# Kernel tuning notes

Hardware: AMD Instinct MI355X
Metric: run time of the kernel (lower is better)

## Reference

```python
import jax, jax.numpy as jnp
import numpy as np

WS = (2, 7, 7)   # window size (d, h, w)
NH = 4           # num heads
EPS = 1e-5       # LayerNorm eps (torch default)


def _rel_index():
    wd, wh, ww = WS
    coords = np.stack(np.meshgrid(np.arange(wd), np.arange(wh), np.arange(ww), indexing='ij'))  # (3,wd,wh,ww)
    cf = coords.reshape(3, -1)                      # (3, N)
    rel = cf[:, :, None] - cf[:, None, :]           # (3, N, N)
    rel = rel.transpose(1, 2, 0).astype(np.int64)   # (N, N, 3)
    rel[..., 0] += wd - 1
    rel[..., 1] += wh - 1
    rel[..., 2] += ww - 1
    rel[..., 0] *= (2 * wh - 1) * (2 * ww - 1)
    rel[..., 1] *= (2 * ww - 1)
    return jnp.asarray(rel.sum(-1), dtype=jnp.int32)  # (N, N)


def setup_inputs() -> dict:
    key = jax.random.key(0)
    ks = jax.random.split(key, 6)
    C, CH = 128, 512
    TBL = (2 * WS[0] - 1) * (2 * WS[1] - 1) * (2 * WS[2] - 1)  # 507
    rn = lambda k, s, sc=0.02: jax.random.normal(k, s, jnp.float32) * sc
    return {
        'x': jax.random.normal(ks[0], (2, 8, 56, 56, C), jnp.float32),
        'norm1_w': jnp.ones((C,), jnp.float32), 'norm1_b': jnp.zeros((C,), jnp.float32),
        'qkv_w': rn(ks[1], (3 * C, C)), 'qkv_b': jnp.zeros((3 * C,), jnp.float32),
        'bias_table': rn(ks[2], (TBL, NH)),
        'proj_w': rn(ks[3], (C, C)), 'proj_b': jnp.zeros((C,), jnp.float32),
        'norm2_w': jnp.ones((C,), jnp.float32), 'norm2_b': jnp.zeros((C,), jnp.float32),
        'fc1_w': rn(ks[4], (CH, C)), 'fc1_b': jnp.zeros((CH,), jnp.float32),
        'fc2_w': rn(ks[5], (C, CH)), 'fc2_b': jnp.zeros((C,), jnp.float32),
        'rel_index': _rel_index(),
    }


def _layernorm(x, w, b):
    m = jnp.mean(x, axis=-1, keepdims=True)
    v = jnp.mean(jnp.square(x - m), axis=-1, keepdims=True)
    return (x - m) * jax.lax.rsqrt(v + EPS) * w + b


def reference(x, norm1_w, norm1_b, qkv_w, qkv_b, bias_table, proj_w, proj_b,
              norm2_w, norm2_b, fc1_w, fc1_b, fc2_w, fc2_b, rel_index):
    B, D, H, W, C = x.shape
    wd, wh, ww = WS
    N = wd * wh * ww
    hd = C // NH

    shortcut = x
    xn = _layernorm(x, norm1_w, norm1_b)
    # window partition: (B,D,H,W,C) -> (B*nW, N, C)
    xw = xn.reshape(B, D // wd, wd, H // wh, wh, W // ww, ww, C)
    xw = xw.transpose(0, 1, 3, 5, 2, 4, 6, 7).reshape(-1, N, C)
    B_ = xw.shape[0]

    qkv = (xw @ qkv_w.T + qkv_b).reshape(B_, N, 3, NH, hd).transpose(2, 0, 3, 1, 4)
    q, k, v = qkv[0] * (hd ** -0.5), qkv[1], qkv[2]   # (B_, NH, N, hd)
    attn = jnp.einsum('bhnd,bhmd->bhnm', q, k)
    bias = bias_table[rel_index.reshape(-1)].reshape(N, N, NH).transpose(2, 0, 1)  # (NH,N,N)
    attn = jax.nn.softmax(attn + bias[None], axis=-1)
    out = jnp.einsum('bhnm,bhmd->bhnd', attn, v).transpose(0, 2, 1, 3).reshape(B_, N, C)
    out = out @ proj_w.T + proj_b

    # window reverse: (B*nW, N, C) -> (B,D,H,W,C)
    xr = out.reshape(B, D // wd, H // wh, W // ww, wd, wh, ww, C)
    xr = xr.transpose(0, 1, 4, 2, 5, 3, 6, 7).reshape(B, D, H, W, C)

    x = shortcut + xr
    h = _layernorm(x, norm2_w, norm2_b)
    h = jax.nn.gelu(h @ fc1_w.T + fc1_b, approximate=False)  # torch nn.GELU = exact erf
    return x + (h @ fc2_w.T + fc2_b)
```

## Files before the change

### kernel.cpp

```cpp
#include <hip/hip_runtime.h>
#include <hip/hip_bf16.h>

typedef __hip_bfloat16 bf16;
typedef unsigned short u16t;
typedef unsigned int u32t;
typedef __attribute__((ext_vector_type(8))) short bf16x8_t;
typedef __attribute__((ext_vector_type(4))) float f32x4_t;

#define DEVI static __device__ __forceinline__

DEVI float u2f(u32t bits) { union { u32t u; float f; } v; v.u = bits; return v.f; }
DEVI float bflo(u32t u) { return u2f((u & 0xffffu) << 16); }
DEVI float bfhi(u32t u) { return u2f(u & 0xffff0000u); }
DEVI float sh2f(short s) { return u2f(((u32t)(u16t)s) << 16); }
DEVI float bf2f(bf16 h) { return __bfloat162float(h); }
DEVI bf16 f2bf(float f) { return __float2bfloat16(f); }
DEVI u16t f2bfbits(float f) {
  bf16 h = __float2bfloat16(f);
  union { bf16 h; u16t u; } v; v.h = h; return v.u;
}

DEVI void gl_lds16(const void* g, void* l) {
  __builtin_amdgcn_global_load_lds(
      (const __attribute__((address_space(1))) unsigned int*)g,
      (__attribute__((address_space(3))) unsigned int*)l, 16, 0, 0);
}

#define TOK   50176
#define NWIN  512
#define NTOK  98
#define NHEAD 4
#define HDIM  32

__global__ __launch_bounds__(256) void cvt4_k(
    const float* __restrict__ a, const float* __restrict__ b,
    const float* __restrict__ c, const float* __restrict__ d,
    bf16* __restrict__ o) {
  int i = blockIdx.x * 256 + threadIdx.x;
  const float* s; int off;
  if (i < 49152)       { s = a; off = 0; }
  else if (i < 65536)  { s = b; off = 49152; }
  else if (i < 131072) { s = c; off = 65536; }
  else                 { s = d; off = 131072; }
  o[i] = f2bf(s[i - off]);
}

__global__ __launch_bounds__(256) void bias_k(const float* __restrict__ btab,
                                              const int* __restrict__ relidx,
                                              float* __restrict__ BmatT) {
  int idx = blockIdx.x * 256 + threadIdx.x;
  if (idx < NTOK * NTOK) {
    int i = idx / NTOK, j = idx - i * NTOK;
    int r = relidx[idx] * NHEAD;
#pragma unroll
    for (int h = 0; h < NHEAD; h++)
      BmatT[(size_t)(h * NTOK + j) * 112 + i] = btab[r + h];
  }
}

__global__ __launch_bounds__(256) void ln1_k(
    const float* __restrict__ x, const float* __restrict__ w,
    const float* __restrict__ b, bf16* __restrict__ o)
{
  const int wave = threadIdx.x >> 6, lane = threadIdx.x & 63;
  const int t = blockIdx.x * 4 + wave;
  const int c = lane << 1;
  float2 xv = *(const float2*)(x + (size_t)t * 128 + c);
  float x0 = xv.x, x1 = xv.y;
  float s = x0 + x1, ss = x0 * x0 + x1 * x1;
#pragma unroll
  for (int m = 32; m; m >>= 1) { s += __shfl_xor(s, m); ss += __shfl_xor(ss, m); }
  float mean = s * 0.0078125f;
  float var = ss * 0.0078125f - mean * mean;
  float rstd = rsqrtf(var + 1e-5f);
  float y0 = (x0 - mean) * rstd * w[c]     + b[c];
  float y1 = (x1 - mean) * rstd * w[c + 1] + b[c + 1];
  int wi = t % 56; int r = t / 56;
  int hi_ = r % 56; r /= 56;
  int di = r & 7; int bi = r >> 3;
  int nw = ((bi * 4 + (di >> 1)) * 8 + hi_ / 7) * 8 + wi / 7;
  int n  = ((di & 1) * 7 + hi_ % 7) * 7 + wi % 7;
  u32t ov = ((u32t)f2bfbits(y1) << 16) | (u32t)f2bfbits(y0);
  *(u32t*)((u16t*)o + (size_t)(nw * NTOK + n) * 128 + c) = ov;
}

__global__ __launch_bounds__(256) void ln2_k(
    const bf16* __restrict__ x, const float* __restrict__ w,
    const float* __restrict__ b, bf16* __restrict__ o)
{
  const int wave = threadIdx.x >> 6, lane = threadIdx.x & 63;
  const int t = blockIdx.x * 4 + wave;
  const int c = lane << 1;
  u32t u = *(const u32t*)((const u16t*)x + (size_t)t * 128 + c);
  float x0 = bflo(u), x1 = bfhi(u);
  float s = x0 + x1, ss = x0 * x0 + x1 * x1;
#pragma unroll
  for (int m = 32; m; m >>= 1) { s += __shfl_xor(s, m); ss += __shfl_xor(ss, m); }
  float mean = s * 0.0078125f;
  float var = ss * 0.0078125f - mean * mean;
  float rstd = rsqrtf(var + 1e-5f);
  float y0 = (x0 - mean) * rstd * w[c]     + b[c];
  float y1 = (x1 - mean) * rstd * w[c + 1] + b[c + 1];
  u32t ov = ((u32t)f2bfbits(y1) << 16) | (u32t)f2bfbits(y0);
  *(u32t*)((u16t*)o + (size_t)t * 128 + c) = ov;
}

template <int MODE, int NT16>
__global__ __launch_bounds__(256) void gemm_mfma_k(
    const bf16* __restrict__ A, const bf16* __restrict__ W,
    const float* __restrict__ bias, const float* __restrict__ resX,
    const bf16* __restrict__ resB2, bf16* __restrict__ outB,
    float* __restrict__ outF, int N, int K)
{
  __shared__ short As[128 * 64];
  __shared__ short Bs[NT16 * 16 * 64];
  const int tid = threadIdx.x;
  const int rowBase = blockIdx.y << 7;
  const int colBase = blockIdx.x * (NT16 * 16);
  const int wv = tid >> 6, lane = tid & 63;
  const int q = lane >> 4, r16 = lane & 15;
  const int mB = wv << 5;

  f32x4_t acc[2][NT16];
#pragma unroll
  for (int i = 0; i < 2; i++)
#pragma unroll
    for (int j = 0; j < NT16; j++) acc[i][j] = (f32x4_t){0.f, 0.f, 0.f, 0.f};

  for (int k0 = 0; k0 < K; k0 += 64) {
#pragma unroll
    for (int t = 0; t < 4; t++) {
      int f = tid + (t << 8);
      int row = f >> 3, cs = (f & 7) ^ (row & 7);
      gl_lds16((const u16t*)A + (size_t)(rowBase + row) * K + k0 + (cs << 3),
               &As[f << 3]);
    }
#pragma unroll
    for (int t = 0; t < NT16 / 2; t++) {
      int f = tid + (t << 8);
      int row = f >> 3, cs = (f & 7) ^ (row & 7);
      gl_lds16((const u16t*)W + (size_t)(colBase + row) * K + k0 + (cs << 3),
               &Bs[f << 3]);
    }
    __syncthreads();
#pragma unroll
    for (int ks = 0; ks < 2; ks++) {
      bf16x8_t af[2], bfr[NT16];
#pragma unroll
      for (int mt = 0; mt < 2; mt++) {
        int row = mB + (mt << 4) + r16;
        int ch = ((ks << 2) + q) ^ (row & 7);
        af[mt] = *(const bf16x8_t*)&As[(row << 6) + (ch << 3)];
      }
#pragma unroll
      for (int nt = 0; nt < NT16; nt++) {
        int row = (nt << 4) + r16;
        int ch = ((ks << 2) + q) ^ (row & 7);
        bfr[nt] = *(const bf16x8_t*)&Bs[(row << 6) + (ch << 3)];
      }
#pragma unroll
      for (int mt = 0; mt < 2; mt++)
#pragma unroll
        for (int nt = 0; nt < NT16; nt++)
          acc[mt][nt] = __builtin_amdgcn_mfma_f32_16x16x32_bf16(
              af[mt], bfr[nt], acc[mt][nt], 0, 0, 0);
    }
    __syncthreads();
  }

  float bv[NT16];
#pragma unroll
  for (int nt = 0; nt < NT16; nt++) bv[nt] = bias[colBase + (nt << 4) + r16];

  if (MODE == 3) {
#pragma unroll
    for (int mt = 0; mt < 2; mt++)
#pragma unroll
      for (int reg = 0; reg < 4; reg++) {
        int grow = rowBase + mB + (mt << 4) + (q << 2) + reg;
        size_t ob = (size_t)grow * N;
#pragma unroll
        for (int nt = 0; nt < NT16; nt++) {
          int gcol = colBase + (nt << 4) + r16;
          outF[ob + gcol] = acc[mt][nt][reg] + bv[nt] + bf2f(resB2[ob + gcol]);
        }
      }
    return;
  }

#pragma unroll
  for (int mt = 0; mt < 2; mt++)
#pragma unroll
    for (int reg = 0; reg < 4; reg++) {
      int lrow = mB + (mt << 4) + (q << 2) + reg;
#pragma unroll
      for (int nt = 0; nt < NT16; nt++) {
        float v = acc[mt][nt][reg] + bv[nt];
        if (MODE == 2) v = 0.5f * v * (1.0f + erff(v * 0.70710678118654752f));
        As[(lrow << 6) + (nt << 4) + r16] = (short)f2bfbits(v);
      }
    }
  __syncthreads();
#pragma unroll
  for (int t = 0; t < 4; t++) {
    int f = tid + (t << 8);
    int row = f >> 3, c8 = (f & 7) << 3;
    if (MODE == 1) {
      int grow = rowBase + row;
      int nw = grow / NTOK, n = grow - nw * NTOK;
      int wq = nw & 7, hq = (nw >> 3) & 7, dq = (nw >> 6) & 3, bb = nw >> 8;
      int wr = n % 7; int q7 = n / 7; int hr = q7 % 7, dr = q7 / 7;
      int tt = ((bb * 8 + dq * 2 + dr) * 56 + hq * 7 + hr) * 56 + wq * 7 + wr;
      size_t ob = (size_t)tt * 128 + colBase + c8;
      float4 r0 = *(const float4*)(resX + ob);
      float4 r1 = *(const float4*)(resX + ob + 4);
      const short* cs = &As[(row << 6) + c8];
      u16t pk[8];
      pk[0] = f2bfbits(sh2f(cs[0]) + r0.x); pk[1] = f2bfbits(sh2f(cs[1]) + r0.y);
      pk[2] = f2bfbits(sh2f(cs[2]) + r0.z); pk[3] = f2bfbits(sh2f(cs[3]) + r0.w);
      pk[4] = f2bfbits(sh2f(cs[4]) + r1.x); pk[5] = f2bfbits(sh2f(cs[5]) + r1.y);
      pk[6] = f2bfbits(sh2f(cs[6]) + r1.z); pk[7] = f2bfbits(sh2f(cs[7]) + r1.w);
      *(uint4*)((u16t*)outB + ob) = *(const uint4*)pk;
    } else {
      size_t ob = (size_t)(rowBase + row) * N + colBase + c8;
      *(uint4*)((u16t*)outB + ob) = *(const uint4*)&As[(row << 6) + c8];
    }
  }
}

#define PSTR 136
__global__ __launch_bounds__(256) void attn_mfma_k(
    const bf16* __restrict__ qkv, const float* __restrict__ BmatT,
    bf16* __restrict__ out)
{
  __shared__ short Vt[32 * PSTR];
  __shared__ short Ps[112 * PSTR];
  const int nw = blockIdx.x, h = blockIdx.y;
  const int tid = threadIdx.x;
  const int wv = tid >> 6, lane = tid & 63;
  const int q = lane >> 4, r16 = lane & 15;
  const float scale = 0.17677669529663687f;

  for (int idx = tid; idx < 32 * 38; idx += 256) {
    int d = idx / 38, j = 98 + idx % 38;
    Vt[d * PSTR + j] = 0;
  }
  for (int idx = tid; idx < 112 * 12; idx += 256) {
    int r = idx / 12, c = (idx % 12) << 1;
    *(u32t*)&Ps[r * PSTR + 112 + c] = 0;
  }
  for (int idx = tid; idx < NTOK * 16; idx += 256) {
    int j = idx >> 4, d2 = (idx & 15) << 1;
    u32t uv = *(const u32t*)((const u16t*)qkv +
                             (size_t)(nw * NTOK + j) * 384 + 256 + h * 32 + d2);
    Vt[d2 * PSTR + j] = (short)(uv & 0xffffu);
    Vt[(d2 + 1) * PSTR + j] = (short)(uv >> 16);
  }
  __syncthreads();

  const int mt0 = wv;
  const bool has2 = (wv + 4) < 7;
  const int mt1 = has2 ? wv + 4 : wv;

  int i0 = mt0 * 16 + r16; if (i0 > NTOK - 1) i0 = NTOK - 1;
  int i1 = mt1 * 16 + r16; if (i1 > NTOK - 1) i1 = NTOK - 1;
  bf16x8_t aq0 = *(const bf16x8_t*)((const u16t*)qkv +
      (size_t)(nw * NTOK + i0) * 384 + h * 32 + (q << 3));
  bf16x8_t aq1 = *(const bf16x8_t*)((const u16t*)qkv +
      (size_t)(nw * NTOK + i1) * 384 + h * 32 + (q << 3));

  f32x4_t sc[2][7];
#pragma unroll
  for (int nt = 0; nt < 7; nt++) {
    int j = (nt << 4) + r16; if (j > NTOK - 1) j = NTOK - 1;
    bf16x8_t bk = *(const bf16x8_t*)((const u16t*)qkv +
        (size_t)(nw * NTOK + j) * 384 + 128 + h * 32 + (q << 3));
    sc[0][nt] = __builtin_amdgcn_mfma_f32_16x16x32_bf16(
        aq0, bk, (f32x4_t){0.f, 0.f, 0.f, 0.f}, 0, 0, 0);
    sc[1][nt] = __builtin_amdgcn_mfma_f32_16x16x32_bf16(
        aq1, bk, (f32x4_t){0.f, 0.f, 0.f, 0.f}, 0, 0, 0);
  }

#pragma unroll
  for (int sel = 0; sel < 2; sel++) {
    if (sel == 1 && !has2) break;
    int mtile = sel ? mt1 : mt0;
    int ibase = mtile * 16 + (q << 2);
    float s[4][7];
#pragma unroll
    for (int nt = 0; nt < 7; nt++) {
      int j = (nt << 4) + r16;
      int jc = j > NTOK - 1 ? NTOK - 1 : j;
      float4 bT = *(const float4*)&BmatT[(size_t)(h * NTOK + jc) * 112 + ibase];
      float bTa[4] = {bT.x, bT.y, bT.z, bT.w};
#pragma unroll
      for (int reg = 0; reg < 4; reg++) {
        int i = ibase + reg;
        float v = sc[sel][nt][reg] * scale;
        s[reg][nt] = (i < NTOK && j < NTOK) ? v + bTa[reg] : -1.0e30f;
      }
    }
#pragma unroll
    for (int reg = 0; reg < 4; reg++) {
      float m = -3.0e38f;
#pragma unroll
      for (int nt = 0; nt < 7; nt++) m = fmaxf(m, s[reg][nt]);
#pragma unroll
      for (int d = 8; d; d >>= 1) m = fmaxf(m, __shfl_xor(m, d));
      float sum = 0.f;
#pragma unroll
      for (int nt = 0; nt < 7; nt++) { s[reg][nt] = __expf(s[reg][nt] - m); sum += s[reg][nt]; }
#pragma unroll
      for (int d = 8; d; d >>= 1) sum += __shfl_xor(sum, d);
      float inv = 1.f / sum;
#pragma unroll
      for (int nt = 0; nt < 7; nt++)
        Ps[(ibase + reg) * PSTR + (nt << 4) + r16] =
            (short)f2bfbits(s[reg][nt] * inv);
    }
    f32x4_t o0 = {0.f, 0.f, 0.f, 0.f}, o1 = {0.f, 0.f, 0.f, 0.f};
#pragma unroll
    for (int kt = 0; kt < 4; kt++) {
      bf16x8_t ap = *(const bf16x8_t*)&Ps[(mtile * 16 + r16) * PSTR + (kt << 5) + (q << 3)];
      bf16x8_t bv0 = *(const bf16x8_t*)&Vt[r16 * PSTR + (kt << 5) + (q << 3)];
      bf16x8_t bv1 = *(const bf16x8_t*)&Vt[(16 + r16) * PSTR + (kt << 5) + (q << 3)];
      o0 = __builtin_amdgcn_mfma_f32_16x16x32_bf16(ap, bv0, o0, 0, 0, 0);
      o1 = __builtin_amdgcn_mfma_f32_16x16x32_bf16(ap, bv1, o1, 0, 0, 0);
    }
#pragma unroll
    for (int reg = 0; reg < 4; reg++) {
      int i = mtile * 16 + (q << 2) + reg;
      if (i < NTOK) {
        size_t ob = (size_t)(nw * NTOK + i) * 128 + h * 32;
        out[ob + r16] = f2bf(o0[reg]);
        out[ob + 16 + r16] = f2bf(o1[reg]);
      }
    }
  }
}

extern "C" void kernel_launch(void* const* d_in, const int* in_sizes, int n_in,
                              void* d_out, int out_size, void* d_ws, size_t ws_size,
                              hipStream_t stream) {
  const float* x      = (const float*)d_in[0];
  const float* n1w    = (const float*)d_in[1];
  const float* n1b    = (const float*)d_in[2];
  const float* qkv_w  = (const float*)d_in[3];
  const float* qkv_b  = (const float*)d_in[4];
  const float* btab   = (const float*)d_in[5];
  const float* proj_w = (const float*)d_in[6];
  const float* proj_b = (const float*)d_in[7];
  const float* n2w    = (const float*)d_in[8];
  const float* n2b    = (const float*)d_in[9];
  const float* fc1_w  = (const float*)d_in[10];
  const float* fc1_b  = (const float*)d_in[11];
  const float* fc2_w  = (const float*)d_in[12];
  const float* fc2_b  = (const float*)d_in[13];
  const int*   relidx = (const int*)d_in[14];

  const size_t Asz = (size_t)TOK * 128 * 2;
  char* ws = (char*)d_ws;
  bf16* wbf   = (bf16*)ws;
  bf16* qkvw16  = wbf;
  bf16* projw16 = wbf + 49152;
  bf16* fc1w16  = wbf + 65536;
  bf16* fc2w16  = wbf + 131072;
  float* BmatT = (float*)(ws + 393216);
  char* R = ws + (1 << 20);
  bf16* xw    = (bf16*)d_out;
  bf16* attn  = (bf16*)d_out;
  bf16* qkv   = (bf16*)R;
  bf16* x2    = (bf16*)R;
  bf16* xn2   = (bf16*)(R + Asz);
  bf16* hmid  = (bf16*)(R + 2 * Asz);
  float* out  = (float*)d_out;
  const bool fullM = ws_size >= ((size_t)(1 << 20) + 6 * Asz);

  cvt4_k<<<768, 256, 0, stream>>>(qkv_w, proj_w, fc1_w, fc2_w, wbf);
  bias_k<<<38, 256, 0, stream>>>(btab, relidx, BmatT);
  ln1_k<<<TOK / 4, 256, 0, stream>>>(x, n1w, n1b, xw);
  gemm_mfma_k<0, 4><<<dim3(6, TOK / 128), 256, 0, stream>>>(
      xw, qkvw16, qkv_b, nullptr, nullptr, qkv, nullptr, 384, 128);
  attn_mfma_k<<<dim3(NWIN, NHEAD), 256, 0, stream>>>(qkv, BmatT, attn);
  gemm_mfma_k<1, 4><<<dim3(2, TOK / 128), 256, 0, stream>>>(
      attn, projw16, proj_b, x, nullptr, x2, nullptr, 128, 128);
  ln2_k<<<TOK / 4, 256, 0, stream>>>(x2, n2w, n2b, xn2);
  if (fullM) {
    gemm_mfma_k<2, 4><<<dim3(8, TOK / 128), 256, 0, stream>>>(
        xn2, fc1w16, fc1_b, nullptr, nullptr, hmid, nullptr, 512, 128);
    gemm_mfma_k<3, 8><<<dim3(1, TOK / 128), 256, 0, stream>>>(
        hmid, fc2w16, fc2_b, nullptr, x2, nullptr, out, 128, 512);
  } else {
    const int MC = TOK / 4;
    for (int c = 0; c < 4; c++) {
      gemm_mfma_k<2, 4><<<dim3(8, MC / 128), 256, 0, stream>>>(
          xn2 + (size_t)c * MC * 128, fc1w16, fc1_b, nullptr, nullptr,
          hmid, nullptr, 512, 128);
      gemm_mfma_k<3, 4><<<dim3(2, MC / 128), 256, 0, stream>>>(
          hmid, fc2w16, fc2_b, nullptr, x2 + (size_t)c * MC * 128,
          nullptr, out + (size_t)c * MC * 128, 128, 512);
    }
  }
}
```

Baseline: 238.5 us.

## Restructure GEMM: load weights into registers, 128-wide K tiles, staged fp32 epilogue

Rewrites the MFMA GEMM kernel so each wave loads its weight fragments straight from global memory into registers instead of staging them in shared memory. A-tiles are now 128-wide in K with a 16-way XOR swizzle, and the K loop is fully unrolled. The fc2 GEMM moves from a single 128-column block per row tile to two 64-column blocks. Its epilogue now stages fp32 results in LDS so the residual add and output can use coalesced float4 stores. The intent is to cut LDS traffic, reduce barriers and improve store coalescing. In exchange, register pressure goes up (64 bf16x8 weight fragments for the K=512 case), and the A-tile is re-read by twice as many blocks for fc2.

```diff
diff --git a/kernel.cpp b/kernel.cpp
--- a/kernel.cpp
+++ b/kernel.cpp
@@ -105,86 +105,94 @@
   *(u32t*)((u16t*)o + (size_t)t * 128 + c) = ov;
 }
 
-template <int MODE, int NT16>
-__global__ __launch_bounds__(256) void gemm_mfma_k(
+template <int MODE, int KT>
+__global__ __launch_bounds__(256) void gemm2_k(
     const bf16* __restrict__ A, const bf16* __restrict__ W,
     const float* __restrict__ bias, const float* __restrict__ resX,
     const bf16* __restrict__ resB2, bf16* __restrict__ outB,
-    float* __restrict__ outF, int N, int K)
+    float* __restrict__ outF, int N)
 {
-  __shared__ short As[128 * 64];
-  __shared__ short Bs[NT16 * 16 * 64];
+  __shared__ __align__(16) short As[128 * 128];
+  const int K = KT * 128;
   const int tid = threadIdx.x;
   const int rowBase = blockIdx.y << 7;
-  const int colBase = blockIdx.x * (NT16 * 16);
+  const int colBase = blockIdx.x << 6;
   const int wv = tid >> 6, lane = tid & 63;
   const int q = lane >> 4, r16 = lane & 15;
   const int mB = wv << 5;
 
-  f32x4_t acc[2][NT16];
+  f32x4_t acc[2][4];
 #pragma unroll
   for (int i = 0; i < 2; i++)
 #pragma unroll
-    for (int j = 0; j < NT16; j++) acc[i][j] = (f32x4_t){0.f, 0.f, 0.f, 0.f};
-
-  for (int k0 = 0; k0 < K; k0 += 64) {
-#pragma unroll
-    for (int t = 0; t < 4; t++) {
+    for (int j = 0; j < 4; j++) acc[i][j] = (f32x4_t){0.f, 0.f, 0.f, 0.f};
+
+#pragma unroll
+  for (int kt = 0; kt < KT; kt++) {
+    const int kc = kt << 7;
+    bf16x8_t bfr[4][4];
+#pragma unroll
+    for (int nt = 0; nt < 4; nt++)
+#pragma unroll
+      for (int ks = 0; ks < 4; ks++)
+        bfr[nt][ks] = *(const bf16x8_t*)((const u16t*)W +
+            (size_t)(colBase + (nt << 4) + r16) * K + kc + (ks << 5) + (q << 3));
+#pragma unroll
+    for (int t = 0; t < 8; t++) {
       int f = tid + (t << 8);
-      int row = f >> 3, cs = (f & 7) ^ (row & 7);
-      gl_lds16((const u16t*)A + (size_t)(rowBase + row) * K + k0 + (cs << 3),
+      int row = f >> 4, cs = (f & 15) ^ (row & 15);
+      gl_lds16((const u16t*)A + (size_t)(rowBase + row) * K + kc + (cs << 3),
                &As[f << 3]);
     }
-#pragma unroll
-    for (int t = 0; t < NT16 / 2; t++) {
-      int f = tid + (t << 8);
-      int row = f >> 3, cs = (f & 7) ^ (row & 7);
-      gl_lds16((const u16t*)W + (size_t)(colBase + row) * K + k0 + (cs << 3),
-               &Bs[f << 3]);
-    }
     __syncthreads();
 #pragma unroll
-    for (int ks = 0; ks < 2; ks++) {
-      bf16x8_t af[2], bfr[NT16];
+    for (int ks = 0; ks < 4; ks++) {
+      bf16x8_t af[2];
 #pragma unroll
       for (int mt = 0; mt < 2; mt++) {
         int row = mB + (mt << 4) + r16;
-        int ch = ((ks << 2) + q) ^ (row & 7);
-        af[mt] = *(const bf16x8_t*)&As[(row << 6) + (ch << 3)];
+        int slot = ((ks << 2) + q) ^ (row & 15);
+        af[mt] = *(const bf16x8_t*)&As[(row << 7) + (slot << 3)];
       }
 #pragma unroll
-      for (int nt = 0; nt < NT16; nt++) {
-        int row = (nt << 4) + r16;
-        int ch = ((ks << 2) + q) ^ (row & 7);
-        bfr[nt] = *(const bf16x8_t*)&Bs[(row << 6) + (ch << 3)];
+      for (int mt = 0; mt < 2; mt++)
+#pragma unroll
+        for (int nt = 0; nt < 4; nt++)
+          acc[mt][nt] = __builtin_amdgcn_mfma_f32_16x16x32_bf16(
+              af[mt], bfr[nt][ks], acc[mt][nt], 0, 0, 0);
+    }
+    __syncthreads();
+  }
+
+  float bv[4];
+#pragma unroll
+  for (int nt = 0; nt < 4; nt++) bv[nt] = bias[colBase + (nt << 4) + r16];
+
+  if (MODE == 3) {
+    float* Cf = (float*)As;
+#pragma unroll
+    for (int mt = 0; mt < 2; mt++)
+#pragma unroll
+      for (int reg = 0; reg < 4; reg++) {
+        int lrow = mB + (mt << 4) + (q << 2) + reg;
+#pragma unroll
+        for (int nt = 0; nt < 4; nt++)
+          Cf[(lrow << 6) + (nt << 4) + r16] = acc[mt][nt][reg] + bv[nt];
       }
-#pragma unroll
-      for (int mt = 0; mt < 2; mt++)
-#pragma unroll
-        for (int nt = 0; nt < NT16; nt++)
-          acc[mt][nt] = __builtin_amdgcn_mfma_f32_16x16x32_bf16(
-              af[mt], bfr[nt], acc[mt][nt], 0, 0, 0);
-    }
     __syncthreads();
-  }
-
-  float bv[NT16];
-#pragma unroll
-  for (int nt = 0; nt < NT16; nt++) bv[nt] = bias[colBase + (nt << 4) + r16];
-
-  if (MODE == 3) {
-#pragma unroll
-    for (int mt = 0; mt < 2; mt++)
-#pragma unroll
-      for (int reg = 0; reg < 4; reg++) {
-        int grow = rowBase + mB + (mt << 4) + (q << 2) + reg;
-        size_t ob = (size_t)grow * N;
-#pragma unroll
-        for (int nt = 0; nt < NT16; nt++) {
-          int gcol = colBase + (nt << 4) + r16;
-          outF[ob + gcol] = acc[mt][nt][reg] + bv[nt] + bf2f(resB2[ob + gcol]);
-        }
-      }
+#pragma unroll
+    for (int t = 0; t < 8; t++) {
+      int f = tid + (t << 8);
+      int row = f >> 4, c4 = (f & 15) << 2;
+      size_t ob = (size_t)(rowBase + row) * N + colBase + c4;
+      const u16t* rp = (const u16t*)resB2 + ob;
+      float4 v;
+      v.x = Cf[(row << 6) + c4]     + sh2f(rp[0]);
+      v.y = Cf[(row << 6) + c4 + 1] + sh2f(rp[1]);
+      v.z = Cf[(row << 6) + c4 + 2] + sh2f(rp[2]);
+      v.w = Cf[(row << 6) + c4 + 3] + sh2f(rp[3]);
+      *(float4*)(outF + ob) = v;
+    }
     return;
   }
 
@@ -194,7 +202,7 @@
     for (int reg = 0; reg < 4; reg++) {
       int lrow = mB + (mt << 4) + (q << 2) + reg;
 #pragma unroll
-      for (int nt = 0; nt < NT16; nt++) {
+      for (int nt = 0; nt < 4; nt++) {
         float v = acc[mt][nt][reg] + bv[nt];
         if (MODE == 2) v = 0.5f * v * (1.0f + erff(v * 0.70710678118654752f));
         As[(lrow << 6) + (nt << 4) + r16] = (short)f2bfbits(v);
@@ -379,26 +387,26 @@
   cvt4_k<<<768, 256, 0, stream>>>(qkv_w, proj_w, fc1_w, fc2_w, wbf);
   bias_k<<<38, 256, 0, stream>>>(btab, relidx, BmatT);
   ln1_k<<<TOK / 4, 256, 0, stream>>>(x, n1w, n1b, xw);
-  gemm_mfma_k<0, 4><<<dim3(6, TOK / 128), 256, 0, stream>>>(
-      xw, qkvw16, qkv_b, nullptr, nullptr, qkv, nullptr, 384, 128);
+  gemm2_k<0, 1><<<dim3(6, TOK / 128), 256, 0, stream>>>(
+      xw, qkvw16, qkv_b, nullptr, nullptr, qkv, nullptr, 384);
   attn_mfma_k<<<dim3(NWIN, NHEAD), 256, 0, stream>>>(qkv, BmatT, attn);
-  gemm_mfma_k<1, 4><<<dim3(2, TOK / 128), 256, 0, stream>>>(
-      attn, projw16, proj_b, x, nullptr, x2, nullptr, 128, 128);
+  gemm2_k<1, 1><<<dim3(2, TOK / 128), 256, 0, stream>>>(
+      attn, projw16, proj_b, x, nullptr, x2, nullptr, 128);
   ln2_k<<<TOK / 4, 256, 0, stream>>>(x2, n2w, n2b, xn2);
   if (fullM) {
-    gemm_mfma_k<2, 4><<<dim3(8, TOK / 128), 256, 0, stream>>>(
-        xn2, fc1w16, fc1_b, nullptr, nullptr, hmid, nullptr, 512, 128);
-    gemm_mfma_k<3, 8><<<dim3(1, TOK / 128), 256, 0, stream>>>(
-        hmid, fc2w16, fc2_b, nullptr, x2, nullptr, out, 128, 512);
+    gemm2_k<2, 1><<<dim3(8, TOK / 128), 256, 0, stream>>>(
+        xn2, fc1w16, fc1_b, nullptr, nullptr, hmid, nullptr, 512);
+    gemm2_k<3, 4><<<dim3(2, TOK / 128), 256, 0, stream>>>(
+        hmid, fc2w16, fc2_b, nullptr, x2, nullptr, out, 128);
   } else {
     const int MC = TOK / 4;
     for (int c = 0; c < 4; c++) {
-      gemm_mfma_k<2, 4><<<dim3(8, MC / 128), 256, 0, stream>>>(
+      gemm2_k<2, 1><<<dim3(8, MC / 128), 256, 0, stream>>>(
           xn2 + (size_t)c * MC * 128, fc1w16, fc1_b, nullptr, nullptr,
-          hmid, nullptr, 512, 128);
-      gemm_mfma_k<3, 4><<<dim3(2, MC / 128), 256, 0, stream>>>(
+          hmid, nullptr, 512);
+      gemm2_k<3, 4><<<dim3(2, MC / 128), 256, 0, stream>>>(
           hmid, fc2w16, fc2_b, nullptr, x2 + (size_t)c * MC * 128,
-          nullptr, out + (size_t)c * MC * 128, 128, 512);
-    }
-  }
-}
+          nullptr, out + (size_t)c * MC * 128, 128);
+    }
+  }
+}
```

Result: slower. 278.1 us (+16.6%).
